# Kernel optimization log

Measured on AMD Instinct MI355X. Metric: run time of the kernel, lower is better.

## Reference

```python
import jax, jax.numpy as jnp
import numpy as np

N, E, FIN, HID, TDIM, HEADS, G = 40000, 1000000, 128, 128, 16, 4, 64
C = HID // HEADS  # per-head channels = 32
NEG_SLOPE = 0.2
LN_EPS = 1e-5


def _layernorm(v, w, b):
    mu = jnp.mean(v, axis=-1, keepdims=True)
    var = jnp.var(v, axis=-1, keepdims=True)
    return (v - mu) * jax.lax.rsqrt(var + LN_EPS) * w + b


def _gat(h, src, dst, w, att_s, att_d, bias):
    # h: [N, Din]; w: [HEADS*C, Din]; att_s/att_d: [HEADS, C]
    xh = (h @ w.T).reshape(N, HEADS, C)                      # [N, HEADS, C]
    a_src = jnp.sum(xh * att_s, axis=-1)                     # [N, HEADS]
    a_dst = jnp.sum(xh * att_d, axis=-1)                     # [N, HEADS]
    e = a_src[src] + a_dst[dst]                              # [E2, HEADS]
    e = jnp.where(e > 0, e, NEG_SLOPE * e)                   # leaky_relu
    m = jax.ops.segment_max(e, dst, num_segments=N)          # [N, HEADS]
    e = jnp.exp(e - jax.lax.stop_gradient(m)[dst])
    denom = jax.ops.segment_sum(e, dst, num_segments=N)      # [N, HEADS]
    alpha = e / denom[dst]                                   # softmax over in-edges
    msg = xh[src] * alpha[..., None]                         # [E2, HEADS, C]
    out = jax.ops.segment_sum(msg, dst, num_segments=N)      # [N, HEADS, C]
    return out.reshape(N, HEADS * C) + bias


def setup_inputs() -> dict:
    key = jax.random.key(0)
    ks = jax.random.split(key, 24)
    s = lambda d: 1.0 / np.sqrt(d)
    inp = {
        "x": jax.random.normal(ks[0], (N, FIN), jnp.float32),
        "edge_index": jax.random.randint(ks[1], (2, E), 0, N, jnp.int64),
        "timestamps": jax.random.uniform(ks[2], (E,), jnp.float32) * 100.0,
        "batch": (jnp.arange(N, dtype=jnp.int64) * G) // N,
        "time_w": jax.random.normal(ks[3], (TDIM, 1), jnp.float32),
        "time_b": jax.random.normal(ks[4], (TDIM,), jnp.float32) * 0.1,
        "proj_w": jax.random.normal(ks[5], (HID, FIN), jnp.float32) * s(FIN),
        "proj_b": jnp.zeros((HID,), jnp.float32),
        "gat0_w": jax.random.normal(ks[6], (HEADS * C, HID + TDIM), jnp.float32) * s(HID + TDIM),
        "att_src0": jax.random.normal(ks[7], (HEADS, C), jnp.float32) * s(C),
        "att_dst0": jax.random.normal(ks[8], (HEADS, C), jnp.float32) * s(C),
        "gat0_b": jnp.zeros((HID,), jnp.float32),
        "ln0_w": jnp.ones((HID,), jnp.float32),
        "ln0_b": jnp.zeros((HID,), jnp.float32),
        "gat1_w": jax.random.normal(ks[9], (HEADS * C, HID), jnp.float32) * s(HID),
        "att_src1": jax.random.normal(ks[10], (HEADS, C), jnp.float32) * s(C),
        "att_dst1": jax.random.normal(ks[11], (HEADS, C), jnp.float32) * s(C),
        "gat1_b": jnp.zeros((HID,), jnp.float32),
        "ln1_w": jnp.ones((HID,), jnp.float32),
        "ln1_b": jnp.zeros((HID,), jnp.float32),
        "cls_w1": jax.random.normal(ks[12], (HID, 2 * HID), jnp.float32) * s(2 * HID),
        "cls_b1": jnp.zeros((HID,), jnp.float32),
        "cls_w2": jax.random.normal(ks[13], (2, HID), jnp.float32) * s(HID),
        "cls_b2": jnp.zeros((2,), jnp.float32),
    }
    return inp


def reference(x, edge_index, timestamps, batch, time_w, time_b, proj_w, proj_b,
              gat0_w, att_src0, att_dst0, gat0_b, ln0_w, ln0_b,
              gat1_w, att_src1, att_dst1, gat1_b, ln1_w, ln1_b,
              cls_w1, cls_b1, cls_w2, cls_b2):
    src, dst = edge_index[0], edge_index[1]
    # node projection + time-encoding scatter-add onto targets
    h = x @ proj_w.T + proj_b                                # [N, HID]
    t_enc = jnp.cos(timestamps[:, None] * time_w[:, 0] + time_b)  # [E, TDIM]
    t_node = jnp.zeros((N, TDIM), h.dtype).at[dst].add(t_enc)
    h = jnp.concatenate([h, t_node], axis=-1)                # [N, HID+TDIM]
    # add self-loops (PyG GATConv default)
    loop = jnp.arange(N, dtype=src.dtype)
    src2 = jnp.concatenate([src, loop])
    dst2 = jnp.concatenate([dst, loop])
    # layer 0 and layer 1: GAT -> LayerNorm -> ReLU (dropout off in eval)
    h = jax.nn.relu(_layernorm(_gat(h, src2, dst2, gat0_w, att_src0, att_dst0, gat0_b), ln0_w, ln0_b))
    h = jax.nn.relu(_layernorm(_gat(h, src2, dst2, gat1_w, att_src1, att_dst1, gat1_b), ln1_w, ln1_b))
    # graph pooling
    cnt = jax.ops.segment_sum(jnp.ones((N, 1), h.dtype), batch, num_segments=G)
    h_mean = jax.ops.segment_sum(h, batch, num_segments=G) / cnt
    h_max = jax.ops.segment_max(h, batch, num_segments=G)
    hg = jnp.concatenate([h_mean, h_max], axis=-1)           # [G, 2*HID]
    hg = jax.nn.relu(hg @ cls_w1.T + cls_b1)
    return hg @ cls_w2.T + cls_b2                            # [G, 2]
```

## Files before the change

### kernel.cpp

```cpp
#include <hip/hip_runtime.h>
#include <math.h>

static constexpr int kN     = 40000;
static constexpr int kE     = 1000000;
static constexpr int kTDIM  = 16;
static constexpr int kG     = 64;
static constexpr int kPOOLC = 16;
static constexpr int kNB    = (kN + 255) / 256;
static constexpr int kCH    = 2048;
static constexpr int kPB    = (kE + kCH - 1) / kCH;
#define LN_EPS 1e-5f
#define NEG_SLOPE 0.2f

typedef __attribute__((ext_vector_type(8))) short bf16x8;
typedef __attribute__((ext_vector_type(4))) float f32x4;

__device__ __forceinline__ float leaky(float v) {
  return v > 0.f ? v : NEG_SLOPE * v;
}

__device__ __forceinline__ unsigned short f2bf(float f) {
  unsigned u = __float_as_uint(f);
  unsigned r = u + 0x7fffu + ((u >> 16) & 1u);
  return (unsigned short)(r >> 16);
}
__device__ __forceinline__ float bflo(unsigned u) { return __uint_as_float(u << 16); }
__device__ __forceinline__ float bfhi(unsigned u) { return __uint_as_float(u & 0xffff0000u); }

__global__ void k_transpose(const float* __restrict__ w, float* __restrict__ wt,
                            int J, int K) {
  int idx = blockIdx.x * 256 + threadIdx.x;
  if (idx >= J * K) return;
  int j = idx / K, k = idx - j * K;
  wt[k * J + j] = w[idx];
}

__global__ void __launch_bounds__(256) k_x2bf(const float* __restrict__ in,
                                              unsigned short* __restrict__ out,
                                              int total4) {
  int i = blockIdx.x * 256 + threadIdx.x;
  if (i >= total4) return;
  float4 v = *(const float4*)(in + (size_t)i * 4);
  ushort4 o = {f2bf(v.x), f2bf(v.y), f2bf(v.z), f2bf(v.w)};
  *(ushort4*)(out + (size_t)i * 4) = o;
}

__global__ void k_w2bf(const float* __restrict__ w, unsigned short* __restrict__ o,
                       int J, int Kin, int Kpad) {
  int idx = blockIdx.x * 256 + threadIdx.x;
  if (idx >= J * Kpad) return;
  int j = idx / Kpad, k = idx - j * Kpad;
  o[idx] = (k < Kin) ? f2bf(w[j * Kin + k]) : (unsigned short)0;
}

__global__ void __launch_bounds__(256) k_part0(const int* __restrict__ dst,
                                               int* __restrict__ gbhist) {
  __shared__ int h[kNB];
  int t = threadIdx.x;
  for (int i = t; i < kNB; i += 256) h[i] = 0;
  __syncthreads();
  int base = blockIdx.x * kCH;
#pragma unroll
  for (int i = 0; i < kCH / 256; ++i) {
    int e = base + i * 256 + t;
    if (e < kE) atomicAdd(&h[dst[e] >> 8], 1);
  }
  __syncthreads();
  for (int i = t; i < kNB; i += 256) {
    int c = h[i];
    if (c) atomicAdd(gbhist + i, c);
  }
}

__global__ void __launch_bounds__(256) k_bprefix(const int* __restrict__ gbhist,
                                                 int* __restrict__ bucketbase,
                                                 int* __restrict__ gcursor,
                                                 int* __restrict__ rowptr) {
  __shared__ int sh[256];
  int t = threadIdx.x;
  int v = (t < kNB) ? gbhist[t] : 0;
  sh[t] = v;
  __syncthreads();
  for (int off = 1; off < 256; off <<= 1) {
    int a = (t >= off) ? sh[t - off] : 0;
    __syncthreads();
    sh[t] += a;
    __syncthreads();
  }
  int excl = sh[t] - v;
  if (t <= kNB) bucketbase[t] = excl;
  if (t < kNB) gcursor[t] = excl;
  if (t == 0) rowptr[kN] = kE;
}

__global__ void __launch_bounds__(256) k_part1(
    const int* __restrict__ src, const int* __restrict__ dst,
    const float* __restrict__ ts, int* __restrict__ gcursor,
    int2* __restrict__ tmp) {
  __shared__ int hist[kNB];
  __shared__ int lbase[kNB];
  int t = threadIdx.x;
  for (int i = t; i < kNB; i += 256) hist[i] = 0;
  __syncthreads();
  int base = blockIdx.x * kCH;
  int bk[8];
  int2 ent[8];
#pragma unroll
  for (int i = 0; i < 8; ++i) {
    int e = base + i * 256 + t;
    if (e < kE) {
      int d = dst[e];
      int b = d >> 8;
      bk[i] = b;
      ent[i] = make_int2(src[e] | ((d & 255) << 16), __float_as_int(ts[e]));
      atomicAdd(&hist[b], 1);
    } else {
      bk[i] = -1;
    }
  }
  __syncthreads();
  for (int i = t; i < kNB; i += 256) {
    int c = hist[i];
    lbase[i] = c ? atomicAdd(gcursor + i, c) : 0;
  }
  __syncthreads();
  for (int i = t; i < kNB; i += 256) hist[i] = 0;
  __syncthreads();
#pragma unroll
  for (int i = 0; i < 8; ++i) {
    if (bk[i] >= 0) {
      int off = atomicAdd(&hist[bk[i]], 1);
      tmp[lbase[bk[i]] + off] = ent[i];
    }
  }
}

__global__ void __launch_bounds__(256) k_part2(
    const int2* __restrict__ tmp, const int* __restrict__ bucketbase,
    int* __restrict__ rowptr, int2* __restrict__ csr) {
  __shared__ int cnt[256];
  __shared__ int sh[256];
  __shared__ int cur[256];
  int b = blockIdx.x;
  int t = threadIdx.x;
  int lo = bucketbase[b], hi = bucketbase[b + 1];
  int nnode = kN - b * 256;
  nnode = nnode < 256 ? nnode : 256;
  cnt[t] = 0;
  __syncthreads();
  for (int p = lo + t; p < hi; p += 256)
    atomicAdd(&cnt[(tmp[p].x >> 16) & 255], 1);
  __syncthreads();
  int v = cnt[t];
  sh[t] = v;
  __syncthreads();
  for (int off = 1; off < 256; off <<= 1) {
    int a = (t >= off) ? sh[t - off] : 0;
    __syncthreads();
    sh[t] += a;
    __syncthreads();
  }
  int nodebase = lo + sh[t] - v;
  if (t < nnode) rowptr[b * 256 + t] = nodebase;
  cur[t] = nodebase;
  __syncthreads();
  for (int p = lo + t; p < hi; p += 256) {
    int2 e = tmp[p];
    int pos = atomicAdd(&cur[(e.x >> 16) & 255], 1);
    csr[pos] = make_int2(e.x & 0xffff, e.y);
  }
}

__global__ void __launch_bounds__(256) k_time_gather(
    const int* __restrict__ rowptr, const int2* __restrict__ csr,
    const float* __restrict__ tw, const float* __restrict__ tb,
    unsigned short* __restrict__ hb) {
  int n = blockIdx.x * 4 + (threadIdx.x >> 6);
  if (n >= kN) return;
  int lane = threadIdx.x & 63;
  int j = lane & 15, grp = lane >> 4;
  float w = tw[j], b = tb[j];
  int lo = rowptr[n], hi = rowptr[n + 1];
  float s = 0.f;
  for (int p = lo + grp; p < hi; p += 4) {
    s += cosf(__int_as_float(csr[p].y) * w + b);
  }
  s += __shfl_xor(s, 16);
  s += __shfl_xor(s, 32);
  if (grp == 0) hb[(size_t)n * 160 + 128 + j] = f2bf(s);
}

__global__ void __launch_bounds__(256) k_mfma_proj(
    const unsigned short* __restrict__ xb, const unsigned short* __restrict__ wb,
    const float* __restrict__ bias, unsigned short* __restrict__ outb) {
  int n0 = blockIdx.x * 16;
  int wv = threadIdx.x >> 6, l = threadIdx.x & 63;
  int lr = l & 15, lk = l >> 4;
  const int K = 128;
  int jt0 = 2 * wv, jt1 = 2 * wv + 1;
  const unsigned short* arow = xb + (size_t)(n0 + lr) * K + lk * 8;
  const unsigned short* brow0 = wb + (size_t)(jt0 * 16 + lr) * K + lk * 8;
  const unsigned short* brow1 = wb + (size_t)(jt1 * 16 + lr) * K + lk * 8;
  f32x4 acc0 = {0.f, 0.f, 0.f, 0.f}, acc1 = {0.f, 0.f, 0.f, 0.f};
#pragma unroll
  for (int c = 0; c < 4; ++c) {
    bf16x8 a = *(const bf16x8*)(arow + c * 32);
    acc0 = __builtin_amdgcn_mfma_f32_16x16x32_bf16(a, *(const bf16x8*)(brow0 + c * 32), acc0, 0, 0, 0);
    acc1 = __builtin_amdgcn_mfma_f32_16x16x32_bf16(a, *(const bf16x8*)(brow1 + c * 32), acc1, 0, 0, 0);
  }
  int j0 = jt0 * 16 + lr, j1 = jt1 * 16 + lr;
  float bb0 = bias[j0], bb1 = bias[j1];
#pragma unroll
  for (int r = 0; r < 4; ++r) {
    int node = n0 + lk * 4 + r;
    outb[(size_t)node * 160 + j0] = f2bf(acc0[r] + bb0);
    outb[(size_t)node * 160 + j1] = f2bf(acc1[r] + bb1);
  }
}

__global__ void __launch_bounds__(256) k_mfma_xh_att(
    const unsigned short* __restrict__ hb, int K,
    const unsigned short* __restrict__ wb,
    const float* __restrict__ att_s, const float* __restrict__ att_d,
    unsigned short* __restrict__ xh, float* __restrict__ a_src,
    float* __restrict__ a_dst) {
  int n0 = blockIdx.x * 16;
  int wv = threadIdx.x >> 6, l = threadIdx.x & 63;
  int lr = l & 15, lk = l >> 4;
  int jt0 = 2 * wv, jt1 = 2 * wv + 1;
  const unsigned short* arow = hb + (size_t)(n0 + lr) * K + lk * 8;
  const unsigned short* brow0 = wb + (size_t)(jt0 * 16 + lr) * K + lk * 8;
  const unsigned short* brow1 = wb + (size_t)(jt1 * 16 + lr) * K + lk * 8;
  f32x4 acc0 = {0.f, 0.f, 0.f, 0.f}, acc1 = {0.f, 0.f, 0.f, 0.f};
  int nch = K >> 5;
  for (int c = 0; c < nch; ++c) {
    bf16x8 a = *(const bf16x8*)(arow + c * 32);
    acc0 = __builtin_amdgcn_mfma_f32_16x16x32_bf16(a, *(const bf16x8*)(brow0 + c * 32), acc0, 0, 0, 0);
    acc1 = __builtin_amdgcn_mfma_f32_16x16x32_bf16(a, *(const bf16x8*)(brow1 + c * 32), acc1, 0, 0, 0);
  }
  int j0 = jt0 * 16 + lr, j1 = jt1 * 16 + lr;
  float as0 = att_s[j0], as1 = att_s[j1];
  float ad0 = att_d[j0], ad1 = att_d[j1];
#pragma unroll
  for (int r = 0; r < 4; ++r) {
    int node = n0 + lk * 4 + r;
    float d0 = acc0[r], d1 = acc1[r];
    xh[(size_t)node * 128 + j0] = f2bf(d0);
    xh[(size_t)node * 128 + j1] = f2bf(d1);
    float vs = d0 * as0 + d1 * as1;
    float vd = d0 * ad0 + d1 * ad1;
    vs += __shfl_xor(vs, 1); vs += __shfl_xor(vs, 2);
    vs += __shfl_xor(vs, 4); vs += __shfl_xor(vs, 8);
    vd += __shfl_xor(vd, 1); vd += __shfl_xor(vd, 2);
    vd += __shfl_xor(vd, 4); vd += __shfl_xor(vd, 8);
    if (lr == 0) {
      a_src[node * 4 + wv] = vs;
      a_dst[node * 4 + wv] = vd;
    }
  }
}

__global__ void __launch_bounds__(256) k_gat_agg(
    const unsigned short* __restrict__ xh, const float* __restrict__ a_src,
    const float* __restrict__ a_dst,
    const int* __restrict__ rowptr, const int2* __restrict__ csr,
    const float* __restrict__ gb, const float* __restrict__ lw,
    const float* __restrict__ lb, unsigned short* __restrict__ outb) {
  int n = blockIdx.x * 4 + (threadIdx.x >> 6);
  if (n >= kN) return;
  int lane = threadIdx.x & 63;
  int eg = lane >> 4;
  int li = lane & 15;
  int hd = li >> 2;
  float ad = a_dst[n * 4 + hd];

  float den = 0.f;
  float a0 = 0.f, a1 = 0.f, a2 = 0.f, a3 = 0.f, a4 = 0.f, a5 = 0.f, a6 = 0.f, a7 = 0.f;

  if (eg == 0) {
    float w_self = __expf(leaky(a_src[n * 4 + hd] + ad));
    den = w_self;
    uint4 u = ((const uint4*)(xh + (size_t)n * 128))[li];
    a0 = w_self * bflo(u.x); a1 = w_self * bfhi(u.x);
    a2 = w_self * bflo(u.y); a3 = w_self * bfhi(u.y);
    a4 = w_self * bflo(u.z); a5 = w_self * bfhi(u.z);
    a6 = w_self * bflo(u.w); a7 = w_self * bfhi(u.w);
  }

  int lo = rowptr[n], hi = rowptr[n + 1];
#pragma unroll 2
  for (int p = lo; p < hi; p += 4) {
    int e = p + eg;
    if (e < hi) {
      int s = csr[e].x;
      float wv = __expf(leaky(a_src[s * 4 + hd] + ad));
      uint4 u = ((const uint4*)(xh + (size_t)s * 128))[li];
      den += wv;
      a0 += wv * bflo(u.x); a1 += wv * bfhi(u.x);
      a2 += wv * bflo(u.y); a3 += wv * bfhi(u.y);
      a4 += wv * bflo(u.z); a5 += wv * bfhi(u.z);
      a6 += wv * bflo(u.w); a7 += wv * bfhi(u.w);
    }
  }

#pragma unroll
  for (int off = 16; off <= 32; off <<= 1) {
    den += __shfl_xor(den, off);
    a0 += __shfl_xor(a0, off); a1 += __shfl_xor(a1, off);
    a2 += __shfl_xor(a2, off); a3 += __shfl_xor(a3, off);
    a4 += __shfl_xor(a4, off); a5 += __shfl_xor(a5, off);
    a6 += __shfl_xor(a6, off); a7 += __shfl_xor(a7, off);
  }

  float inv = 1.f / den;
  int c0 = li * 8;
  float4 gbl = *(const float4*)(gb + c0);
  float4 gbh = *(const float4*)(gb + c0 + 4);
  float v0 = a0 * inv + gbl.x, v1 = a1 * inv + gbl.y;
  float v2 = a2 * inv + gbl.z, v3 = a3 * inv + gbl.w;
  float v4 = a4 * inv + gbh.x, v5 = a5 * inv + gbh.y;
  float v6 = a6 * inv + gbh.z, v7 = a7 * inv + gbh.w;
  float s = v0 + v1 + v2 + v3 + v4 + v5 + v6 + v7;
  float sq = v0*v0 + v1*v1 + v2*v2 + v3*v3 + v4*v4 + v5*v5 + v6*v6 + v7*v7;
#pragma unroll
  for (int off = 1; off <= 8; off <<= 1) {
    s += __shfl_xor(s, off);
    sq += __shfl_xor(sq, off);
  }
  float mean = s * (1.f / 128.f);
  float var = sq * (1.f / 128.f) - mean * mean;
  float rs = rsqrtf(var + LN_EPS);
  if (eg == 0) {
    float4 lwl = *(const float4*)(lw + c0), lwh = *(const float4*)(lw + c0 + 4);
    float4 lbl = *(const float4*)(lb + c0), lbh = *(const float4*)(lb + c0 + 4);
    float y0 = fmaxf((v0 - mean) * rs * lwl.x + lbl.x, 0.f);
    float y1 = fmaxf((v1 - mean) * rs * lwl.y + lbl.y, 0.f);
    float y2 = fmaxf((v2 - mean) * rs * lwl.z + lbl.z, 0.f);
    float y3 = fmaxf((v3 - mean) * rs * lwl.w + lbl.w, 0.f);
    float y4 = fmaxf((v4 - mean) * rs * lwh.x + lbh.x, 0.f);
    float y5 = fmaxf((v5 - mean) * rs * lwh.y + lbh.y, 0.f);
    float y6 = fmaxf((v6 - mean) * rs * lwh.z + lbh.z, 0.f);
    float y7 = fmaxf((v7 - mean) * rs * lwh.w + lbh.w, 0.f);
    uint4 o;
    o.x = (unsigned)f2bf(y0) | ((unsigned)f2bf(y1) << 16);
    o.y = (unsigned)f2bf(y2) | ((unsigned)f2bf(y3) << 16);
    o.z = (unsigned)f2bf(y4) | ((unsigned)f2bf(y5) << 16);
    o.w = (unsigned)f2bf(y6) | ((unsigned)f2bf(y7) << 16);
    *(uint4*)(outb + (size_t)n * 128 + c0) = o;
  }
}

__global__ void __launch_bounds__(128) k_pool1(
    const unsigned short* __restrict__ h, const int* __restrict__ batch,
    float* __restrict__ psum, float* __restrict__ pmax) {
  int g = blockIdx.x >> 4, chunk = blockIdx.x & (kPOOLC - 1);
  int c = threadIdx.x;
  int lo, hi;
  { int a = 0, b = kN; while (a < b) { int m = (a + b) >> 1; if (batch[m] < g) a = m + 1; else b = m; } lo = a; }
  { int a = 0, b = kN; while (a < b) { int m = (a + b) >> 1; if (batch[m] < g + 1) a = m + 1; else b = m; } hi = a; }
  int len = hi - lo;
  int c0 = lo + (int)(((long long)len * chunk) / kPOOLC);
  int c1 = lo + (int)(((long long)len * (chunk + 1)) / kPOOLC);
  float s = 0.f, mx = -INFINITY;
  for (int n = c0; n < c1; ++n) {
    float v = __uint_as_float(((unsigned)h[(size_t)n * 128 + c]) << 16);
    s += v;
    mx = fmaxf(mx, v);
  }
  psum[(size_t)blockIdx.x * 128 + c] = s;
  pmax[(size_t)blockIdx.x * 128 + c] = mx;
}

__global__ void __launch_bounds__(128) k_pool2_cls(
    const float* __restrict__ psum, const float* __restrict__ pmax,
    const int* __restrict__ batch,
    const float* __restrict__ w1t, const float* __restrict__ b1,
    const float* __restrict__ w2, const float* __restrict__ b2,
    float* __restrict__ out) {
  __shared__ float row[256];
  __shared__ float o1[128];
  int g = blockIdx.x;
  int c = threadIdx.x;
  int lo, hi;
  { int a = 0, b = kN; while (a < b) { int m = (a + b) >> 1; if (batch[m] < g) a = m + 1; else b = m; } lo = a; }
  { int a = 0, b = kN; while (a < b) { int m = (a + b) >> 1; if (batch[m] < g + 1) a = m + 1; else b = m; } hi = a; }
  float s = 0.f, mx = -INFINITY;
#pragma unroll
  for (int k = 0; k < kPOOLC; ++k) {
    s += psum[(size_t)(g * kPOOLC + k) * 128 + c];
    mx = fmaxf(mx, pmax[(size_t)(g * kPOOLC + k) * 128 + c]);
  }
  int cnt = hi - lo;
  row[c] = (cnt > 0) ? s / (float)cnt : 0.f;
  row[c + 128] = mx;
  __syncthreads();
  float t = b1[c];
  for (int k = 0; k < 256; ++k) t += row[k] * w1t[k * 128 + c];
  o1[c] = fmaxf(t, 0.f);
  __syncthreads();
  if (c < 2) {
    float r = b2[c];
    for (int j = 0; j < 128; ++j) r += o1[j] * w2[c * 128 + j];
    out[g * 2 + c] = r;
  }
}

extern "C" void kernel_launch(void* const* d_in, const int* in_sizes, int n_in,
                              void* d_out, int out_size, void* d_ws, size_t ws_size,
                              hipStream_t stream) {
  const float* x      = (const float*)d_in[0];
  const int*   ei     = (const int*)d_in[1];
  const float* ts     = (const float*)d_in[2];
  const int*   batch  = (const int*)d_in[3];
  const float* time_w = (const float*)d_in[4];
  const float* time_b = (const float*)d_in[5];
  const float* proj_w = (const float*)d_in[6];
  const float* proj_b = (const float*)d_in[7];
  const float* g0w    = (const float*)d_in[8];
  const float* as0    = (const float*)d_in[9];
  const float* ad0    = (const float*)d_in[10];
  const float* g0b    = (const float*)d_in[11];
  const float* ln0w   = (const float*)d_in[12];
  const float* ln0b   = (const float*)d_in[13];
  const float* g1w    = (const float*)d_in[14];
  const float* as1    = (const float*)d_in[15];
  const float* ad1    = (const float*)d_in[16];
  const float* g1b    = (const float*)d_in[17];
  const float* ln1w   = (const float*)d_in[18];
  const float* ln1b   = (const float*)d_in[19];
  const float* c1w    = (const float*)d_in[20];
  const float* c1b    = (const float*)d_in[21];
  const float* c2w    = (const float*)d_in[22];
  const float* c2b    = (const float*)d_in[23];
  float* out = (float*)d_out;

  const int* src = ei;
  const int* dst = ei + kE;

  char* p = (char*)d_ws;
  unsigned short* xh   = (unsigned short*)p; p += (size_t)kN * 128 * 2;
  unsigned short* hb16 = (unsigned short*)p; p += (size_t)kN * 160 * 2;
  unsigned short* h1b16= (unsigned short*)p; p += (size_t)kN * 128 * 2;
  float* a_src = (float*)p; p += (size_t)kN * 4 * 4;
  float* a_dst = (float*)p; p += (size_t)kN * 4 * 4;
  unsigned short* pwb = (unsigned short*)p; p += 128 * 128 * 2;
  unsigned short* w0b = (unsigned short*)p; p += 128 * 160 * 2;
  unsigned short* w1b = (unsigned short*)p; p += 128 * 128 * 2;
  float* c1T = (float*)p; p += 256 * 128 * 4;
  int2* csr = (int2*)p; p += (size_t)kE * 8;
  int2* tmp = (int2*)p; p += (size_t)kE * 8;
  float* psum = (float*)p; p += (size_t)kG * kPOOLC * 128 * 4;
  float* pmax = (float*)p; p += (size_t)kG * kPOOLC * 128 * 4;
  int* rowptr = (int*)p; p += (kN + 1) * 4;
  int* gbhist = (int*)p; p += kNB * 4;
  int* bucketbase = (int*)p; p += (kNB + 1) * 4;
  int* gcursor = (int*)p; p += kNB * 4;
  unsigned short* xb16 = xh;

  k_transpose<<<(128 * 256 + 255) / 256, 256, 0, stream>>>(c1w, c1T, 128, 256);
  k_w2bf<<<(128 * 128 + 255) / 256, 256, 0, stream>>>(proj_w, pwb, 128, 128, 128);
  k_w2bf<<<(128 * 160 + 255) / 256, 256, 0, stream>>>(g0w, w0b, 128, 144, 160);
  k_w2bf<<<(128 * 128 + 255) / 256, 256, 0, stream>>>(g1w, w1b, 128, 128, 128);

  hipMemsetAsync(gbhist, 0, kNB * sizeof(int), stream);
  k_part0<<<kPB, 256, 0, stream>>>(dst, gbhist);
  k_bprefix<<<1, 256, 0, stream>>>(gbhist, bucketbase, gcursor, rowptr);
  k_part1<<<kPB, 256, 0, stream>>>(src, dst, ts, gcursor, tmp);
  k_part2<<<kNB, 256, 0, stream>>>(tmp, bucketbase, rowptr, csr);

  k_x2bf<<<(kN * 128 / 4 + 255) / 256, 256, 0, stream>>>(x, xb16, kN * 128 / 4);
  hipMemsetAsync(hb16, 0, (size_t)kN * 160 * 2, stream);
  k_mfma_proj<<<kN / 16, 256, 0, stream>>>(xb16, pwb, proj_b, hb16);
  k_time_gather<<<kN / 4, 256, 0, stream>>>(rowptr, csr, time_w, time_b, hb16);

  k_mfma_xh_att<<<kN / 16, 256, 0, stream>>>(hb16, 160, w0b, as0, ad0, xh, a_src, a_dst);
  k_gat_agg<<<kN / 4, 256, 0, stream>>>(xh, a_src, a_dst, rowptr, csr,
                                        g0b, ln0w, ln0b, h1b16);

  k_mfma_xh_att<<<kN / 16, 256, 0, stream>>>(h1b16, 128, w1b, as1, ad1, xh, a_src, a_dst);
  k_gat_agg<<<kN / 4, 256, 0, stream>>>(xh, a_src, a_dst, rowptr, csr,
                                        g1b, ln1w, ln1b, h1b16);

  k_pool1<<<kG * kPOOLC, 128, 0, stream>>>(h1b16, batch, psum, pmax);
  k_pool2_cls<<<kG, 128, 0, stream>>>(psum, pmax, batch, c1T, c1b, c2w, c2b, out);
}
```

Before: 285.6 us.

## Fuse prep kernels, fold x-to-bf16 into projection, add nontemporal memory hints

Merges the weight transpose, three weight bf16 conversions and the histogram zeroing into a single prep kernel. The projection now reads fp32 x directly and converts it in registers, so the separate conversion kernel and the full memset of the hidden buffer go away; the padding columns are zeroed in the time-gather kernel instead. It also adds nontemporal loads and stores for the partition temp buffer, CSR reads, GAT output and pooling reads, raises the unroll factor in the aggregation loop, and writes leaky ReLU as fmaxf. Together these cut launch count and memory traffic, at the cost of some extra conversion ALU in the projection and possible cache-policy side effects.

```diff
diff --git a/kernel.cpp b/kernel.cpp
--- a/kernel.cpp
+++ b/kernel.cpp
@@ -14,9 +14,10 @@
 
 typedef __attribute__((ext_vector_type(8))) short bf16x8;
 typedef __attribute__((ext_vector_type(4))) float f32x4;
+typedef __attribute__((ext_vector_type(4))) unsigned uv4;
 
 __device__ __forceinline__ float leaky(float v) {
-  return v > 0.f ? v : NEG_SLOPE * v;
+  return fmaxf(v, NEG_SLOPE * v);
 }
 
 __device__ __forceinline__ unsigned short f2bf(float f) {
@@ -27,30 +28,34 @@
 __device__ __forceinline__ float bflo(unsigned u) { return __uint_as_float(u << 16); }
 __device__ __forceinline__ float bfhi(unsigned u) { return __uint_as_float(u & 0xffff0000u); }
 
-__global__ void k_transpose(const float* __restrict__ w, float* __restrict__ wt,
-                            int J, int K) {
+static constexpr int kP0 = 256 * 128;
+static constexpr int kP1 = kP0 + 128 * 128;
+static constexpr int kP2 = kP1 + 128 * 160;
+static constexpr int kP3 = kP2 + 128 * 128;
+static constexpr int kP4 = kP3 + kNB;
+__global__ void __launch_bounds__(256) k_prep(
+    const float* __restrict__ c1w, float* __restrict__ c1T,
+    const float* __restrict__ pw, unsigned short* __restrict__ pwb,
+    const float* __restrict__ g0w, unsigned short* __restrict__ w0b,
+    const float* __restrict__ g1w, unsigned short* __restrict__ w1b,
+    int* __restrict__ gbhist) {
   int idx = blockIdx.x * 256 + threadIdx.x;
-  if (idx >= J * K) return;
-  int j = idx / K, k = idx - j * K;
-  wt[k * J + j] = w[idx];
-}
-
-__global__ void __launch_bounds__(256) k_x2bf(const float* __restrict__ in,
-                                              unsigned short* __restrict__ out,
-                                              int total4) {
-  int i = blockIdx.x * 256 + threadIdx.x;
-  if (i >= total4) return;
-  float4 v = *(const float4*)(in + (size_t)i * 4);
-  ushort4 o = {f2bf(v.x), f2bf(v.y), f2bf(v.z), f2bf(v.w)};
-  *(ushort4*)(out + (size_t)i * 4) = o;
-}
-
-__global__ void k_w2bf(const float* __restrict__ w, unsigned short* __restrict__ o,
-                       int J, int Kin, int Kpad) {
-  int idx = blockIdx.x * 256 + threadIdx.x;
-  if (idx >= J * Kpad) return;
-  int j = idx / Kpad, k = idx - j * Kpad;
-  o[idx] = (k < Kin) ? f2bf(w[j * Kin + k]) : (unsigned short)0;
+  if (idx < kP0) {
+    int j = idx / 256, k = idx - j * 256;
+    c1T[k * 128 + j] = c1w[idx];
+  } else if (idx < kP1) {
+    int i = idx - kP0;
+    pwb[i] = f2bf(pw[i]);
+  } else if (idx < kP2) {
+    int i = idx - kP1;
+    int j = i / 160, k = i - j * 160;
+    w0b[i] = (k < 144) ? f2bf(g0w[j * 144 + k]) : (unsigned short)0;
+  } else if (idx < kP3) {
+    int i = idx - kP2;
+    w1b[i] = f2bf(g1w[i]);
+  } else if (idx < kP4) {
+    gbhist[idx - kP3] = 0;
+  }
 }
 
 __global__ void __launch_bounds__(256) k_part0(const int* __restrict__ dst,
@@ -96,7 +101,7 @@
 __global__ void __launch_bounds__(256) k_part1(
     const int* __restrict__ src, const int* __restrict__ dst,
     const float* __restrict__ ts, int* __restrict__ gcursor,
-    int2* __restrict__ tmp) {
+    unsigned long long* __restrict__ tmp) {
   __shared__ int hist[kNB];
   __shared__ int lbase[kNB];
   int t = threadIdx.x;
@@ -104,7 +109,7 @@
   __syncthreads();
   int base = blockIdx.x * kCH;
   int bk[8];
-  int2 ent[8];
+  unsigned long long ent[8];
 #pragma unroll
   for (int i = 0; i < 8; ++i) {
     int e = base + i * 256 + t;
@@ -112,7 +117,8 @@
       int d = dst[e];
       int b = d >> 8;
       bk[i] = b;
-      ent[i] = make_int2(src[e] | ((d & 255) << 16), __float_as_int(ts[e]));
+      unsigned lo = (unsigned)src[e] | ((unsigned)(d & 255) << 16);
+      ent[i] = ((unsigned long long)(unsigned)__float_as_int(ts[e]) << 32) | lo;
       atomicAdd(&hist[b], 1);
     } else {
       bk[i] = -1;
@@ -130,13 +136,13 @@
   for (int i = 0; i < 8; ++i) {
     if (bk[i] >= 0) {
       int off = atomicAdd(&hist[bk[i]], 1);
-      tmp[lbase[bk[i]] + off] = ent[i];
+      __builtin_nontemporal_store(ent[i], tmp + lbase[bk[i]] + off);
     }
   }
 }
 
 __global__ void __launch_bounds__(256) k_part2(
-    const int2* __restrict__ tmp, const int* __restrict__ bucketbase,
+    const unsigned long long* __restrict__ tmp, const int* __restrict__ bucketbase,
     int* __restrict__ rowptr, int2* __restrict__ csr) {
   __shared__ int cnt[256];
   __shared__ int sh[256];
@@ -148,8 +154,10 @@
   nnode = nnode < 256 ? nnode : 256;
   cnt[t] = 0;
   __syncthreads();
-  for (int p = lo + t; p < hi; p += 256)
-    atomicAdd(&cnt[(tmp[p].x >> 16) & 255], 1);
+  for (int p = lo + t; p < hi; p += 256) {
+    unsigned long long e = __builtin_nontemporal_load(tmp + p);
+    atomicAdd(&cnt[((unsigned)e >> 16) & 255], 1);
+  }
   __syncthreads();
   int v = cnt[t];
   sh[t] = v;
@@ -165,9 +173,10 @@
   cur[t] = nodebase;
   __syncthreads();
   for (int p = lo + t; p < hi; p += 256) {
-    int2 e = tmp[p];
-    int pos = atomicAdd(&cur[(e.x >> 16) & 255], 1);
-    csr[pos] = make_int2(e.x & 0xffff, e.y);
+    unsigned long long e = __builtin_nontemporal_load(tmp + p);
+    unsigned elo = (unsigned)e;
+    int pos = atomicAdd(&cur[(elo >> 16) & 255], 1);
+    csr[pos] = make_int2((int)(elo & 0xffffu), (int)(unsigned)(e >> 32));
   }
 }
 
@@ -188,23 +197,30 @@
   s += __shfl_xor(s, 16);
   s += __shfl_xor(s, 32);
   if (grp == 0) hb[(size_t)n * 160 + 128 + j] = f2bf(s);
+  if (grp == 1) hb[(size_t)n * 160 + 144 + j] = 0;
 }
 
 __global__ void __launch_bounds__(256) k_mfma_proj(
-    const unsigned short* __restrict__ xb, const unsigned short* __restrict__ wb,
+    const float* __restrict__ x, const unsigned short* __restrict__ wb,
     const float* __restrict__ bias, unsigned short* __restrict__ outb) {
   int n0 = blockIdx.x * 16;
   int wv = threadIdx.x >> 6, l = threadIdx.x & 63;
   int lr = l & 15, lk = l >> 4;
   const int K = 128;
   int jt0 = 2 * wv, jt1 = 2 * wv + 1;
-  const unsigned short* arow = xb + (size_t)(n0 + lr) * K + lk * 8;
+  const float* arow = x + (size_t)(n0 + lr) * K + lk * 8;
   const unsigned short* brow0 = wb + (size_t)(jt0 * 16 + lr) * K + lk * 8;
   const unsigned short* brow1 = wb + (size_t)(jt1 * 16 + lr) * K + lk * 8;
   f32x4 acc0 = {0.f, 0.f, 0.f, 0.f}, acc1 = {0.f, 0.f, 0.f, 0.f};
 #pragma unroll
   for (int c = 0; c < 4; ++c) {
-    bf16x8 a = *(const bf16x8*)(arow + c * 32);
+    float4 alo = *(const float4*)(arow + c * 32);
+    float4 ahi = *(const float4*)(arow + c * 32 + 4);
+    bf16x8 a;
+    a[0] = (short)f2bf(alo.x); a[1] = (short)f2bf(alo.y);
+    a[2] = (short)f2bf(alo.z); a[3] = (short)f2bf(alo.w);
+    a[4] = (short)f2bf(ahi.x); a[5] = (short)f2bf(ahi.y);
+    a[6] = (short)f2bf(ahi.z); a[7] = (short)f2bf(ahi.w);
     acc0 = __builtin_amdgcn_mfma_f32_16x16x32_bf16(a, *(const bf16x8*)(brow0 + c * 32), acc0, 0, 0, 0);
     acc1 = __builtin_amdgcn_mfma_f32_16x16x32_bf16(a, *(const bf16x8*)(brow1 + c * 32), acc1, 0, 0, 0);
   }
@@ -273,6 +289,7 @@
   int li = lane & 15;
   int hd = li >> 2;
   float ad = a_dst[n * 4 + hd];
+  const int* csrx = (const int*)csr;
 
   float den = 0.f;
   float a0 = 0.f, a1 = 0.f, a2 = 0.f, a3 = 0.f, a4 = 0.f, a5 = 0.f, a6 = 0.f, a7 = 0.f;
@@ -288,11 +305,11 @@
   }
 
   int lo = rowptr[n], hi = rowptr[n + 1];
-#pragma unroll 2
+#pragma unroll 4
   for (int p = lo; p < hi; p += 4) {
     int e = p + eg;
     if (e < hi) {
-      int s = csr[e].x;
+      int s = __builtin_nontemporal_load(csrx + 2 * (size_t)e);
       float wv = __expf(leaky(a_src[s * 4 + hd] + ad));
       uint4 u = ((const uint4*)(xh + (size_t)s * 128))[li];
       den += wv;
@@ -341,12 +358,12 @@
     float y5 = fmaxf((v5 - mean) * rs * lwh.y + lbh.y, 0.f);
     float y6 = fmaxf((v6 - mean) * rs * lwh.z + lbh.z, 0.f);
     float y7 = fmaxf((v7 - mean) * rs * lwh.w + lbh.w, 0.f);
-    uint4 o;
+    uv4 o;
     o.x = (unsigned)f2bf(y0) | ((unsigned)f2bf(y1) << 16);
     o.y = (unsigned)f2bf(y2) | ((unsigned)f2bf(y3) << 16);
     o.z = (unsigned)f2bf(y4) | ((unsigned)f2bf(y5) << 16);
     o.w = (unsigned)f2bf(y6) | ((unsigned)f2bf(y7) << 16);
-    *(uint4*)(outb + (size_t)n * 128 + c0) = o;
+    __builtin_nontemporal_store(o, (uv4*)(outb + (size_t)n * 128 + c0));
   }
 }
 
@@ -363,7 +380,8 @@
   int c1 = lo + (int)(((long long)len * (chunk + 1)) / kPOOLC);
   float s = 0.f, mx = -INFINITY;
   for (int n = c0; n < c1; ++n) {
-    float v = __uint_as_float(((unsigned)h[(size_t)n * 128 + c]) << 16);
+    unsigned short hv = __builtin_nontemporal_load(h + (size_t)n * 128 + c);
+    float v = __uint_as_float(((unsigned)hv) << 16);
     s += v;
     mx = fmaxf(mx, v);
   }
@@ -448,29 +466,23 @@
   unsigned short* w1b = (unsigned short*)p; p += 128 * 128 * 2;
   float* c1T = (float*)p; p += 256 * 128 * 4;
   int2* csr = (int2*)p; p += (size_t)kE * 8;
-  int2* tmp = (int2*)p; p += (size_t)kE * 8;
+  unsigned long long* tmp = (unsigned long long*)p; p += (size_t)kE * 8;
   float* psum = (float*)p; p += (size_t)kG * kPOOLC * 128 * 4;
   float* pmax = (float*)p; p += (size_t)kG * kPOOLC * 128 * 4;
   int* rowptr = (int*)p; p += (kN + 1) * 4;
   int* gbhist = (int*)p; p += kNB * 4;
   int* bucketbase = (int*)p; p += (kNB + 1) * 4;
   int* gcursor = (int*)p; p += kNB * 4;
-  unsigned short* xb16 = xh;
-
-  k_transpose<<<(128 * 256 + 255) / 256, 256, 0, stream>>>(c1w, c1T, 128, 256);
-  k_w2bf<<<(128 * 128 + 255) / 256, 256, 0, stream>>>(proj_w, pwb, 128, 128, 128);
-  k_w2bf<<<(128 * 160 + 255) / 256, 256, 0, stream>>>(g0w, w0b, 128, 144, 160);
-  k_w2bf<<<(128 * 128 + 255) / 256, 256, 0, stream>>>(g1w, w1b, 128, 128, 128);
-
-  hipMemsetAsync(gbhist, 0, kNB * sizeof(int), stream);
+
+  k_prep<<<(kP4 + 255) / 256, 256, 0, stream>>>(c1w, c1T, proj_w, pwb, g0w, w0b,
+                                                g1w, w1b, gbhist);
+
   k_part0<<<kPB, 256, 0, stream>>>(dst, gbhist);
   k_bprefix<<<1, 256, 0, stream>>>(gbhist, bucketbase, gcursor, rowptr);
   k_part1<<<kPB, 256, 0, stream>>>(src, dst, ts, gcursor, tmp);
   k_part2<<<kNB, 256, 0, stream>>>(tmp, bucketbase, rowptr, csr);
 
-  k_x2bf<<<(kN * 128 / 4 + 255) / 256, 256, 0, stream>>>(x, xb16, kN * 128 / 4);
-  hipMemsetAsync(hb16, 0, (size_t)kN * 160 * 2, stream);
-  k_mfma_proj<<<kN / 16, 256, 0, stream>>>(xb16, pwb, proj_b, hb16);
+  k_mfma_proj<<<kN / 16, 256, 0, stream>>>(x, pwb, proj_b, hb16);
   k_time_gather<<<kN / 4, 256, 0, stream>>>(rowptr, csr, time_w, time_b, hb16);
 
   k_mfma_xh_att<<<kN / 16, 256, 0, stream>>>(hb16, 160, w0b, as0, ad0, xh, a_src, a_dst);
```

After: 316.4 us. 1.11x slower.
